# Optimization experiments

Measured on AMD Instinct MI355X. Metric: run time of the kernel, lower is better.

The kernel has to match this reference:

```python
import jax, jax.numpy as jnp
import numpy as np

HIDDEN = 896   # GRU size
HALF = HIDDEN // 2
BINS = 256     # 2 ** (16 / 2)
T = 16384      # signal length (timesteps)
INV_BINS = 1.0 / ((BINS - 1) / 2.0)


def setup_inputs() -> dict:
    key = jax.random.key(0)
    ks = jax.random.split(key, 14)
    s = 0.05
    return {
        "project_hidden_weight": jax.random.normal(ks[0], (3 * HIDDEN, HIDDEN), jnp.float32) * s,
        "project_hidden_bias": jax.random.normal(ks[1], (3 * HIDDEN,), jnp.float32) * s,
        "project_coarse_weight": jax.random.normal(ks[2], (3 * HALF, 2), jnp.float32) * s,
        "project_fine_weight": jax.random.normal(ks[3], (3 * HALF, 3), jnp.float32) * s,
        "project_coarse_bias": jax.random.normal(ks[4], (T, 3 * HALF), jnp.float32) * s,
        "project_fine_bias": jax.random.normal(ks[5], (T, 3 * HALF), jnp.float32) * s,
        "to_bins_coarse_pre_weight": jax.random.normal(ks[6], (HALF, HALF), jnp.float32) * s,
        "to_bins_coarse_pre_bias": jax.random.normal(ks[7], (HALF,), jnp.float32) * s,
        "to_bins_coarse_weight": jax.random.normal(ks[8], (BINS, HALF), jnp.float32) * s,
        "to_bins_coarse_bias": jax.random.normal(ks[9], (BINS,), jnp.float32) * s,
        "to_bins_fine_pre_weight": jax.random.normal(ks[10], (HALF, HALF), jnp.float32) * s,
        "to_bins_fine_pre_bias": jax.random.normal(ks[11], (HALF,), jnp.float32) * s,
        "to_bins_fine_weight": jax.random.normal(ks[12], (BINS, HALF), jnp.float32) * s,
        "to_bins_fine_bias": jax.random.normal(ks[13], (BINS,), jnp.float32) * s,
        "hidden_state": jnp.zeros((HIDDEN,), jnp.float32),
    }


def _half_step(inp, h, bias_t, W_in, hproj, pre_b, pre_W, bin_b, bin_W):
    # inp: [n], h: [HALF], bias_t/hproj: [3*HALF]
    proj = bias_t + W_in @ inp                               # [3*HALF]
    ri = jax.nn.sigmoid(proj[:2 * HALF] + hproj[:2 * HALF])  # r gate | u gate
    n = jnp.tanh(proj[2 * HALF:] + ri[:HALF] * hproj[2 * HALF:])
    h_new = ri[HALF:] * (h - n) + n                          # u*h + (1-u)*n
    pre = jax.nn.relu(pre_b + pre_W @ h_new)
    logits = bin_b + bin_W @ pre                             # [BINS]
    sample = jnp.argmax(logits).astype(jnp.int32)            # argmax sampling
    return h_new, sample, logits


def reference(project_hidden_weight, project_hidden_bias, project_coarse_weight,
              project_fine_weight, project_coarse_bias, project_fine_bias,
              to_bins_coarse_pre_weight, to_bins_coarse_pre_bias,
              to_bins_coarse_weight, to_bins_coarse_bias,
              to_bins_fine_pre_weight, to_bins_fine_pre_bias,
              to_bins_fine_weight, to_bins_fine_bias, hidden_state):
    init_scaled = jnp.float32((BINS // 2) * INV_BINS - 1.0)

    def step(carry, biases):
        h, c_prev, f_prev = carry
        cb, fb = biases
        hp = project_hidden_bias + project_hidden_weight @ h  # [3*HIDDEN]
        inp_c = jnp.stack([c_prev, f_prev])
        h_c, c_s, _ = _half_step(inp_c, h[:HALF], cb, project_coarse_weight,
                                 hp[:3 * HALF], to_bins_coarse_pre_bias,
                                 to_bins_coarse_pre_weight, to_bins_coarse_bias,
                                 to_bins_coarse_weight)
        c_scaled = c_s.astype(jnp.float32) * INV_BINS - 1.0
        inp_f = jnp.stack([c_prev, f_prev, c_scaled])
        h_f, f_s, _ = _half_step(inp_f, h[HALF:], fb, project_fine_weight,
                                 hp[3 * HALF:], to_bins_fine_pre_bias,
                                 to_bins_fine_pre_weight, to_bins_fine_bias,
                                 to_bins_fine_weight)
        f_scaled = f_s.astype(jnp.float32) * INV_BINS - 1.0
        return (jnp.concatenate([h_c, h_f]), c_scaled, f_scaled), (c_s, f_s)

    init = (hidden_state, init_scaled, init_scaled)
    (h_fin, _, _), (out_c, out_f) = jax.lax.scan(
        step, init, (project_coarse_bias, project_fine_bias))
    return out_c, out_f, h_fin
```

## Files before the change

### kernel.cpp

```cpp
#include <hip/hip_runtime.h>

#define AGENT __HIP_MEMORY_SCOPE_AGENT
typedef unsigned int u32;
typedef unsigned long long u64;

constexpr int TSTEPS = 16384;
constexpr float INV_BINS    = 1.0f / 127.5f;
constexpr float INIT_SCALED = 128.0f * (1.0f / 127.5f) - 1.0f;
constexpr int REP = 4;

constexpr int HT_OFF  = 0;
constexpr int HPT_OFF = 114688;
constexpr int PL_OFF  = 157696;

__device__ __forceinline__ u64  ld64(const u64* p){ return __hip_atomic_load((u64*)p, __ATOMIC_RELAXED, AGENT); }
__device__ __forceinline__ void st64(u64* p, u64 v){ __hip_atomic_store(p, v, __ATOMIC_RELAXED, AGENT); }

__device__ __forceinline__ float wave_sum(float s) {
  #pragma unroll
  for (int d = 1; d < 64; d <<= 1) s += __shfl_xor(s, d, 64);
  return s;
}
__device__ __forceinline__ u64 u64max(u64 a, u64 b) { return a > b ? a : b; }
__device__ __forceinline__ u64 wave_max64(u64 v) {
  #pragma unroll
  for (int d = 1; d < 64; d <<= 1) v = u64max(v, __shfl_xor(v, d, 64));
  return v;
}
__device__ __forceinline__ float sigf(float x) { return 1.0f / (1.0f + __expf(-x)); }
__device__ __forceinline__ u64  tagf(u32 tg, float x) { return ((u64)tg << 32) | (u64)__float_as_uint(x); }
__device__ __forceinline__ u32  tago(u64 v) { return (u32)(v >> 32); }
__device__ __forceinline__ float valf(u64 v) { return __uint_as_float((u32)(v & 0xFFFFFFFFull)); }

__device__ __forceinline__ u64 amkey(float x, int row) {
  u32 u = __float_as_uint(x);
  u = (u & 0x80000000u) ? ~u : (u | 0x80000000u);
  return ((u64)u << 8) | (u64)(u32)(255 - row);
}
__device__ __forceinline__ int amrow(u64 k) { return 255 - (int)(k & 0xFFull); }

extern "C" __global__ void __launch_bounds__(256, 1)
wavernn_persist(const float* __restrict__ Wh,  const float* __restrict__ bh,
                const float* __restrict__ Wci, const float* __restrict__ Wfi,
                const float* __restrict__ cbias, const float* __restrict__ fbias,
                const float* __restrict__ pWc, const float* __restrict__ pBc,
                const float* __restrict__ bWc, const float* __restrict__ bBc,
                const float* __restrict__ pWf, const float* __restrict__ pBf,
                const float* __restrict__ bWf, const float* __restrict__ bBf,
                const float* __restrict__ h0,
                float* __restrict__ out, char* __restrict__ wsb)
{
  const int tid  = threadIdx.x;
  const int lane = tid & 63;
  const int wv   = tid >> 6;
  const int wg   = blockIdx.x;

  u64* HT  = (u64*)(wsb + HT_OFF);
  u64* HPT = (u64*)(wsb + HPT_OFF);
  u64* PL  = (u64*)(wsb + PL_OFF);

  if (wg < 32) {
    const int half = wg >> 4;
    const int oid  = wg & 15;
    const int ncol = half ? 3 : 2;
    const float* Wi  = half ? Wfi : Wci;
    const float* tbp = half ? fbias : cbias;
    const float* pW  = half ? pWf : pWc;
    const float* pB  = half ? pBf : pBc;
    const float* bW  = half ? bWf : bWc;
    const float* bB  = half ? bBf : bBc;

    const int u1 = tid;
    const bool hasB = (tid < 192);
    const int u2 = 256 + tid;

    float wiA[3][3], wiB[3][3];
    #pragma unroll
    for (int g = 0; g < 3; ++g)
      #pragma unroll
      for (int c = 0; c < 3; ++c) {
        wiA[g][c] = (c < ncol) ? Wi[(g * 448 + u1) * ncol + c] : 0.0f;
        wiB[g][c] = (hasB && c < ncol) ? Wi[(g * 448 + u2) * ncol + c] : 0.0f;
      }
    float hvA = h0[half * 448 + u1];
    float hvB = hasB ? h0[half * 448 + u2] : 0.0f;

    float wpre[7][7], bpre[7];
    #pragma unroll
    for (int r = 0; r < 7; ++r) {
      const int row = oid * 28 + wv * 7 + r;
      #pragma unroll
      for (int k = 0; k < 7; ++k) wpre[r][k] = pW[row * 448 + k * 64 + lane];
      bpre[r] = pB[row];
    }
    float wbin[28];
    #pragma unroll
    for (int j = 0; j < 28; ++j) wbin[j] = bW[tid * 448 + oid * 28 + j];
    const float bbin = (oid == 0) ? bB[tid] : 0.0f;

    __shared__ float sh[448];
    __shared__ float spre[28];
    __shared__ u64 smA[4], smB[4], smX[4];

    for (int t = 0; t < TSTEPS; ++t) {
      const int par = t & 1;
      const u32 tg  = (u32)(t + 1);

      float tbA[3], tbB[3];
      #pragma unroll
      for (int g = 0; g < 3; ++g) {
        tbA[g] = tbp[(size_t)t * 1344 + g * 448 + u1];
        tbB[g] = hasB ? tbp[(size_t)t * 1344 + g * 448 + u2] : 0.0f;
      }

      float c_prev, f_prev;
      if (t >= 1) {
        const int parp = par ^ 1;
        const u64* plc = PL + (size_t)((parp * 2 + 0) * 16) * 256 + tid;
        const u64* plf = PL + (size_t)((parp * 2 + 1) * 16) * 256 + tid;
        float sc = 0.f, sf = 0.f;
        for (;;) {
          u64 vc[16], vf[16]; bool ok = true;
          #pragma unroll
          for (int o = 0; o < 16; ++o) { vc[o] = ld64(plc + o * 256); ok &= (tago(vc[o]) == (u32)t); }
          #pragma unroll
          for (int o = 0; o < 16; ++o) { vf[o] = ld64(plf + o * 256); ok &= (tago(vf[o]) == (u32)t); }
          if (__all(ok)) {
            sc = 0.f; sf = 0.f;
            #pragma unroll
            for (int o = 0; o < 16; ++o) { sc += valf(vc[o]); sf += valf(vf[o]); }
            break;
          }
        }
        const u64 kc = wave_max64(amkey(sc, tid));
        const u64 kf = wave_max64(amkey(sf, tid));
        if (lane == 0) { smA[wv] = kc; smB[wv] = kf; }
        __syncthreads();
        const u64 mc = u64max(u64max(smA[0], smA[1]), u64max(smA[2], smA[3]));
        const u64 mf = u64max(u64max(smB[0], smB[1]), u64max(smB[2], smB[3]));
        c_prev = (float)amrow(mc) * INV_BINS - 1.0f;
        f_prev = (float)amrow(mf) * INV_BINS - 1.0f;
        if (!half && oid == 0 && tid == 0) out[TSTEPS + t - 1] = (float)amrow(mf);
      } else {
        c_prev = INIT_SCALED; f_prev = INIT_SCALED;
      }

      const u64* hpt = HPT + (size_t)(par * 2 + half) * 1344;
      float hpA[3], hpB[3];
      for (;;) {
        u64 a0 = ld64(hpt + u1), a1 = ld64(hpt + 448 + u1), a2 = ld64(hpt + 896 + u1);
        u64 b0 = 0, b1 = 0, b2 = 0;
        bool ok = (tago(a0) == tg) && (tago(a1) == tg) && (tago(a2) == tg);
        if (hasB) {
          b0 = ld64(hpt + u2); b1 = ld64(hpt + 448 + u2); b2 = ld64(hpt + 896 + u2);
          ok &= (tago(b0) == tg) && (tago(b1) == tg) && (tago(b2) == tg);
        }
        if (__all(ok)) {
          hpA[0] = valf(a0); hpA[1] = valf(a1); hpA[2] = valf(a2);
          hpB[0] = valf(b0); hpB[1] = valf(b1); hpB[2] = valf(b2);
          break;
        }
      }

      float in2A[3], in2B[3];
      if (!half) {
        #pragma unroll
        for (int g = 0; g < 3; ++g) {
          in2A[g] = fmaf(wiA[g][1], f_prev, fmaf(wiA[g][0], c_prev, tbA[g]));
          in2B[g] = fmaf(wiB[g][1], f_prev, fmaf(wiB[g][0], c_prev, tbB[g]));
        }
      } else {
        const u64* plc = PL + (size_t)((par * 2 + 0) * 16) * 256 + tid;
        float sc2;
        for (;;) {
          u64 v[16]; bool ok = true;
          #pragma unroll
          for (int o = 0; o < 16; ++o) { v[o] = ld64(plc + o * 256); ok &= (tago(v[o]) == tg); }
          if (__all(ok)) {
            sc2 = 0.f;
            #pragma unroll
            for (int o = 0; o < 16; ++o) sc2 += valf(v[o]);
            break;
          }
        }
        const u64 k = wave_max64(amkey(sc2, tid));
        if (lane == 0) smX[wv] = k;
        __syncthreads();
        const u64 m = u64max(u64max(smX[0], smX[1]), u64max(smX[2], smX[3]));
        const int cbin = amrow(m);
        const float csc = (float)cbin * INV_BINS - 1.0f;
        if (oid == 0 && tid == 0) out[t] = (float)cbin;
        #pragma unroll
        for (int g = 0; g < 3; ++g) {
          in2A[g] = fmaf(wiA[g][2], csc, fmaf(wiA[g][1], f_prev, fmaf(wiA[g][0], c_prev, tbA[g])));
          in2B[g] = fmaf(wiB[g][2], csc, fmaf(wiB[g][1], f_prev, fmaf(wiB[g][0], c_prev, tbB[g])));
        }
      }

      {
        const float r = sigf(in2A[0] + hpA[0]);
        const float u = sigf(in2A[1] + hpA[1]);
        const float n = tanhf(in2A[2] + r * hpA[2]);
        hvA = u * (hvA - n) + n;
        sh[u1] = hvA;
        if (oid < REP) st64(HT + ((size_t)((par * 2 + half) * REP + oid)) * 448 + u1, tagf(tg, hvA));
      }
      if (hasB) {
        const float r = sigf(in2B[0] + hpB[0]);
        const float u = sigf(in2B[1] + hpB[1]);
        const float n = tanhf(in2B[2] + r * hpB[2]);
        hvB = u * (hvB - n) + n;
        sh[u2] = hvB;
        if (oid < REP) st64(HT + ((size_t)((par * 2 + half) * REP + oid)) * 448 + u2, tagf(tg, hvB));
      }
      __syncthreads();

      {
        float hv7[7];
        #pragma unroll
        for (int k = 0; k < 7; ++k) hv7[k] = sh[k * 64 + lane];
        #pragma unroll
        for (int r = 0; r < 7; ++r) {
          float s = 0.f;
          #pragma unroll
          for (int k = 0; k < 7; ++k) s = fmaf(wpre[r][k], hv7[k], s);
          s = fmaxf(wave_sum(s) + bpre[r], 0.f);
          if (lane == 0) spre[wv * 7 + r] = s;
        }
      }
      __syncthreads();

      {
        float pl = bbin;
        #pragma unroll
        for (int j = 0; j < 28; ++j) pl = fmaf(wbin[j], spre[j], pl);
        st64(PL + ((size_t)((par * 2 + half) * 16 + oid)) * 256 + tid, tagf(tg, pl));
      }
    }

    if (!half && oid == 0) {
      const u64* plf = PL + (size_t)((1 * 2 + 1) * 16) * 256 + tid;
      float sf;
      for (;;) {
        u64 v[16]; bool ok = true;
        #pragma unroll
        for (int o = 0; o < 16; ++o) { v[o] = ld64(plf + o * 256); ok &= (tago(v[o]) == 16384u); }
        if (__all(ok)) {
          sf = 0.f;
          #pragma unroll
          for (int o = 0; o < 16; ++o) sf += valf(v[o]);
          break;
        }
      }
      const u64 k = wave_max64(amkey(sf, tid));
      if (lane == 0) smA[wv] = k;
      __syncthreads();
      if (tid == 0)
        out[2 * TSTEPS - 1] =
            (float)amrow(u64max(u64max(smA[0], smA[1]), u64max(smA[2], smA[3])));
    }
    if (oid == 0) {
      out[2 * TSTEPS + half * 448 + u1] = hvA;
      if (hasB) out[2 * TSTEPS + half * 448 + u2] = hvB;
    }

  } else {
    const int id   = wg - 32;
    const int half = (id >= 42) ? 1 : 0;
    const int wgl  = id - 42 * half;
    const int r0   = (wgl * 4 + wv) * 8;
    const int rep  = wg & (REP - 1);

    float wh[8][14], hb[8];
    #pragma unroll
    for (int j = 0; j < 8; ++j) {
      const int grow = half * 1344 + r0 + j;
      #pragma unroll
      for (int k = 0; k < 14; ++k) wh[j][k] = Wh[(size_t)grow * 896 + k * 64 + lane];
      hb[j] = bh[grow];
    }

    for (int t = 0; t < TSTEPS; ++t) {
      const int par = t & 1;
      const u32 tg  = (u32)(t + 1);
      float s[8];

      if (t == 0) {
        float hv[14];
        #pragma unroll
        for (int k = 0; k < 14; ++k) hv[k] = h0[k * 64 + lane];
        #pragma unroll
        for (int j = 0; j < 8; ++j) {
          float a = 0.f;
          #pragma unroll
          for (int k = 0; k < 14; ++k) a = fmaf(wh[j][k], hv[k], a);
          s[j] = a;
        }
      } else {
        const u32 tp = (u32)t;
        const int p2 = (par ^ 1) * 2;
        const u64* hc = HT + ((size_t)((p2 + 0) * REP + rep)) * 448 + lane;
        const u64* hf = HT + ((size_t)((p2 + 1) * REP + rep)) * 448 + lane;
        {
          float hv[7];
          for (;;) {
            u64 v[7]; bool ok = true;
            #pragma unroll
            for (int k = 0; k < 7; ++k) { v[k] = ld64(hc + k * 64); ok &= (tago(v[k]) == tp); }
            if (__all(ok)) {
              #pragma unroll
              for (int k = 0; k < 7; ++k) hv[k] = valf(v[k]);
              break;
            }
          }
          #pragma unroll
          for (int j = 0; j < 8; ++j) {
            float a = 0.f;
            #pragma unroll
            for (int k = 0; k < 7; ++k) a = fmaf(wh[j][k], hv[k], a);
            s[j] = a;
          }
        }
        for (;;) { u64 sv = ld64(hf + 384); if (__all(tago(sv) == tp)) break; }
        {
          float hv[7];
          for (;;) {
            u64 v[7]; bool ok = true;
            #pragma unroll
            for (int k = 0; k < 7; ++k) { v[k] = ld64(hf + k * 64); ok &= (tago(v[k]) == tp); }
            if (__all(ok)) {
              #pragma unroll
              for (int k = 0; k < 7; ++k) hv[k] = valf(v[k]);
              break;
            }
          }
          #pragma unroll
          for (int j = 0; j < 8; ++j) {
            float a = s[j];
            #pragma unroll
            for (int k = 0; k < 7; ++k) a = fmaf(wh[j][k + 7], hv[k], a);
            s[j] = a;
          }
        }
      }

      u64* hp = HPT + (size_t)(par * 2 + half) * 1344 + r0;
      #pragma unroll
      for (int j = 0; j < 8; ++j) {
        const float a = wave_sum(s[j]) + hb[j];
        if (lane == 0) st64(hp + j, tagf(tg, a));
      }
    }
  }
}

extern "C" void kernel_launch(void* const* d_in, const int* in_sizes, int n_in,
                              void* d_out, int out_size, void* d_ws, size_t ws_size,
                              hipStream_t stream) {
  (void)in_sizes; (void)n_in; (void)out_size; (void)ws_size;
  wavernn_persist<<<116, 256, 0, stream>>>(
      (const float*)d_in[0],  (const float*)d_in[1],  (const float*)d_in[2],
      (const float*)d_in[3],  (const float*)d_in[4],  (const float*)d_in[5],
      (const float*)d_in[6],  (const float*)d_in[7],  (const float*)d_in[8],
      (const float*)d_in[9],  (const float*)d_in[10], (const float*)d_in[11],
      (const float*)d_in[12], (const float*)d_in[13], (const float*)d_in[14],
      (float*)d_out, (char*)d_ws);
}
```

Baseline: 151.1 ms.

## Centralize argmax sampling in dedicated reducer blocks publishing tagged samples

Two extra persistent workgroups now gather the per-step partial logits and compute the coarse and fine argmax. They publish the chosen bin as a tagged 64-bit value that the other 32 GRU workgroups spin on. Before, every GRU block read all 16 partial-logit slices and did its own reduction with block syncs. The partial-logit buffer is transposed so each reducer thread reads 16 contiguous entries, and the hidden-projection blocks first poll one sentinel element before loading the whole hidden vector. This cuts redundant polling and reduction traffic, at the cost of an extra global-memory hop on the serial critical path each timestep.

```diff
diff --git a/kernel.cpp b/kernel.cpp
--- a/kernel.cpp
+++ b/kernel.cpp
@@ -9,9 +9,10 @@
 constexpr float INIT_SCALED = 128.0f * (1.0f / 127.5f) - 1.0f;
 constexpr int REP = 4;
 
-constexpr int HT_OFF  = 0;
-constexpr int HPT_OFF = 114688;
-constexpr int PL_OFF  = 157696;
+constexpr int HT_OFF   = 0;
+constexpr int HPT_OFF  = 114688;
+constexpr int PL_OFF   = 157696;
+constexpr int SAMP_OFF = 288768;
 
 __device__ __forceinline__ u64  ld64(const u64* p){ return __hip_atomic_load((u64*)p, __ATOMIC_RELAXED, AGENT); }
 __device__ __forceinline__ void st64(u64* p, u64 v){ __hip_atomic_store(p, v, __ATOMIC_RELAXED, AGENT); }
@@ -55,9 +56,10 @@
   const int wv   = tid >> 6;
   const int wg   = blockIdx.x;
 
-  u64* HT  = (u64*)(wsb + HT_OFF);
-  u64* HPT = (u64*)(wsb + HPT_OFF);
-  u64* PL  = (u64*)(wsb + PL_OFF);
+  u64* HT   = (u64*)(wsb + HT_OFF);
+  u64* HPT  = (u64*)(wsb + HPT_OFF);
+  u64* PL   = (u64*)(wsb + PL_OFF);
+  u64* SAMP = (u64*)(wsb + SAMP_OFF);
 
   if (wg < 32) {
     const int half = wg >> 4;
@@ -100,7 +102,6 @@
 
     __shared__ float sh[448];
     __shared__ float spre[28];
-    __shared__ u64 smA[4], smB[4], smX[4];
 
     for (int t = 0; t < TSTEPS; ++t) {
       const int par = t & 1;
@@ -116,31 +117,15 @@
       float c_prev, f_prev;
       if (t >= 1) {
         const int parp = par ^ 1;
-        const u64* plc = PL + (size_t)((parp * 2 + 0) * 16) * 256 + tid;
-        const u64* plf = PL + (size_t)((parp * 2 + 1) * 16) * 256 + tid;
-        float sc = 0.f, sf = 0.f;
+        const u64* sc = SAMP + (size_t)((parp * 2 + 0) * 8 + (wg & 7)) * 16;
+        const u64* sf = SAMP + (size_t)((parp * 2 + 1) * 8 + (wg & 7)) * 16;
+        u64 a, b;
         for (;;) {
-          u64 vc[16], vf[16]; bool ok = true;
-          #pragma unroll
-          for (int o = 0; o < 16; ++o) { vc[o] = ld64(plc + o * 256); ok &= (tago(vc[o]) == (u32)t); }
-          #pragma unroll
-          for (int o = 0; o < 16; ++o) { vf[o] = ld64(plf + o * 256); ok &= (tago(vf[o]) == (u32)t); }
-          if (__all(ok)) {
-            sc = 0.f; sf = 0.f;
-            #pragma unroll
-            for (int o = 0; o < 16; ++o) { sc += valf(vc[o]); sf += valf(vf[o]); }
-            break;
-          }
-        }
-        const u64 kc = wave_max64(amkey(sc, tid));
-        const u64 kf = wave_max64(amkey(sf, tid));
-        if (lane == 0) { smA[wv] = kc; smB[wv] = kf; }
-        __syncthreads();
-        const u64 mc = u64max(u64max(smA[0], smA[1]), u64max(smA[2], smA[3]));
-        const u64 mf = u64max(u64max(smB[0], smB[1]), u64max(smB[2], smB[3]));
-        c_prev = (float)amrow(mc) * INV_BINS - 1.0f;
-        f_prev = (float)amrow(mf) * INV_BINS - 1.0f;
-        if (!half && oid == 0 && tid == 0) out[TSTEPS + t - 1] = (float)amrow(mf);
+          a = ld64(sc); b = ld64(sf);
+          if (__all(tago(a) == (u32)t && tago(b) == (u32)t)) break;
+        }
+        c_prev = (float)(u32)(a & 0xFFFFFFFFull) * INV_BINS - 1.0f;
+        f_prev = (float)(u32)(b & 0xFFFFFFFFull) * INV_BINS - 1.0f;
       } else {
         c_prev = INIT_SCALED; f_prev = INIT_SCALED;
       }
@@ -170,30 +155,20 @@
           in2B[g] = fmaf(wiB[g][1], f_prev, fmaf(wiB[g][0], c_prev, tbB[g]));
         }
       } else {
-        const u64* plc = PL + (size_t)((par * 2 + 0) * 16) * 256 + tid;
-        float sc2;
-        for (;;) {
-          u64 v[16]; bool ok = true;
-          #pragma unroll
-          for (int o = 0; o < 16; ++o) { v[o] = ld64(plc + o * 256); ok &= (tago(v[o]) == tg); }
-          if (__all(ok)) {
-            sc2 = 0.f;
-            #pragma unroll
-            for (int o = 0; o < 16; ++o) sc2 += valf(v[o]);
-            break;
-          }
-        }
-        const u64 k = wave_max64(amkey(sc2, tid));
-        if (lane == 0) smX[wv] = k;
-        __syncthreads();
-        const u64 m = u64max(u64max(smX[0], smX[1]), u64max(smX[2], smX[3]));
-        const int cbin = amrow(m);
-        const float csc = (float)cbin * INV_BINS - 1.0f;
-        if (oid == 0 && tid == 0) out[t] = (float)cbin;
+        float linA[3], linB[3];
         #pragma unroll
         for (int g = 0; g < 3; ++g) {
-          in2A[g] = fmaf(wiA[g][2], csc, fmaf(wiA[g][1], f_prev, fmaf(wiA[g][0], c_prev, tbA[g])));
-          in2B[g] = fmaf(wiB[g][2], csc, fmaf(wiB[g][1], f_prev, fmaf(wiB[g][0], c_prev, tbB[g])));
+          linA[g] = fmaf(wiA[g][1], f_prev, fmaf(wiA[g][0], c_prev, tbA[g]));
+          linB[g] = fmaf(wiB[g][1], f_prev, fmaf(wiB[g][0], c_prev, tbB[g]));
+        }
+        const u64* scH = SAMP + (size_t)((par * 2 + 0) * 8 + (oid & 7)) * 16;
+        u64 v;
+        for (;;) { v = ld64(scH); if (__all(tago(v) == tg)) break; }
+        const float csc = (float)(u32)(v & 0xFFFFFFFFull) * INV_BINS - 1.0f;
+        #pragma unroll
+        for (int g = 0; g < 3; ++g) {
+          in2A[g] = fmaf(wiA[g][2], csc, linA[g]);
+          in2B[g] = fmaf(wiB[g][2], csc, linB[g]);
         }
       }
 
@@ -234,34 +209,46 @@
         float pl = bbin;
         #pragma unroll
         for (int j = 0; j < 28; ++j) pl = fmaf(wbin[j], spre[j], pl);
-        st64(PL + ((size_t)((par * 2 + half) * 16 + oid)) * 256 + tid, tagf(tg, pl));
-      }
-    }
-
-    if (!half && oid == 0) {
-      const u64* plf = PL + (size_t)((1 * 2 + 1) * 16) * 256 + tid;
-      float sf;
-      for (;;) {
-        u64 v[16]; bool ok = true;
-        #pragma unroll
-        for (int o = 0; o < 16; ++o) { v[o] = ld64(plf + o * 256); ok &= (tago(v[o]) == 16384u); }
-        if (__all(ok)) {
-          sf = 0.f;
-          #pragma unroll
-          for (int o = 0; o < 16; ++o) sf += valf(v[o]);
-          break;
-        }
-      }
-      const u64 k = wave_max64(amkey(sf, tid));
-      if (lane == 0) smA[wv] = k;
-      __syncthreads();
-      if (tid == 0)
-        out[2 * TSTEPS - 1] =
-            (float)amrow(u64max(u64max(smA[0], smA[1]), u64max(smA[2], smA[3])));
-    }
+        st64(PL + ((size_t)((par * 2 + half) * 256 + tid)) * 16 + oid, tagf(tg, pl));
+      }
+    }
+
     if (oid == 0) {
       out[2 * TSTEPS + half * 448 + u1] = hvA;
       if (hasB) out[2 * TSTEPS + half * 448 + u2] = hvB;
+    }
+
+  } else if (wg >= 116) {
+    const int half = wg - 116;
+    __shared__ u64 sm2[4];
+    for (int t = 0; t < TSTEPS; ++t) {
+      const int par = t & 1;
+      const u32 tg  = (u32)(t + 1);
+      const u64* base = PL + ((size_t)((par * 2 + half) * 256 + tid)) * 16;
+      float s;
+      for (;;) {
+        u64 v0 = ld64(base);
+        if (!__all(tago(v0) == tg)) continue;
+        u64 v[16]; bool ok = true;
+        v[0] = v0;
+        #pragma unroll
+        for (int o = 1; o < 16; ++o) { v[o] = ld64(base + o); ok &= (tago(v[o]) == tg); }
+        if (__all(ok)) {
+          s = 0.f;
+          #pragma unroll
+          for (int o = 0; o < 16; ++o) s += valf(v[o]);
+          break;
+        }
+      }
+      const u64 k = wave_max64(amkey(s, tid));
+      if (lane == 0) sm2[wv] = k;
+      __syncthreads();
+      const u64 m = u64max(u64max(sm2[0], sm2[1]), u64max(sm2[2], sm2[3]));
+      const int bin = amrow(m);
+      if (tid < 8) st64(SAMP + (size_t)((par * 2 + half) * 8 + tid) * 16,
+                        ((u64)tg << 32) | (u32)bin);
+      if (tid == 0) out[half ? (TSTEPS + t) : t] = (float)bin;
+      __syncthreads();
     }
 
   } else {
@@ -301,6 +288,7 @@
         const int p2 = (par ^ 1) * 2;
         const u64* hc = HT + ((size_t)((p2 + 0) * REP + rep)) * 448 + lane;
         const u64* hf = HT + ((size_t)((p2 + 1) * REP + rep)) * 448 + lane;
+        for (;;) { u64 sv = ld64(hc + 384); if (__all(tago(sv) == tp)) break; }
         {
           float hv[7];
           for (;;) {
@@ -358,7 +346,7 @@
                               void* d_out, int out_size, void* d_ws, size_t ws_size,
                               hipStream_t stream) {
   (void)in_sizes; (void)n_in; (void)out_size; (void)ws_size;
-  wavernn_persist<<<116, 256, 0, stream>>>(
+  wavernn_persist<<<118, 256, 0, stream>>>(
       (const float*)d_in[0],  (const float*)d_in[1],  (const float*)d_in[2],
       (const float*)d_in[3],  (const float*)d_in[4],  (const float*)d_in[5],
       (const float*)d_in[6],  (const float*)d_in[7],  (const float*)d_in[8],
```

Result: slower. 219.3 ms (+45.1%).

## Reduce spin-wait contention with sentinel polling, replicated handoff buffers, and register-held coarse sample

Applied to the files above, without the earlier changes.

Polling loops now first spin on a single sentinel word per lane, with s_sleep backoff, before doing the full tagged-vector load. This is meant to cut global memory traffic and contention while blocks wait on each other. The hidden-state replicas go from 4 to 8, and the projected-hidden buffer is duplicated so each pair of workgroups polls its own copy. The fine half reuses its previous coarse sample from a register instead of re-reading and re-reducing the coarse logits, and it precomputes the input terms that do not depend on the current coarse sample. In exchange, the workspace is larger, there are more writers per step, and the sleeps can add wake-up latency.

```diff
diff --git a/kernel.cpp b/kernel.cpp
--- a/kernel.cpp
+++ b/kernel.cpp
@@ -7,11 +7,11 @@
 constexpr int TSTEPS = 16384;
 constexpr float INV_BINS    = 1.0f / 127.5f;
 constexpr float INIT_SCALED = 128.0f * (1.0f / 127.5f) - 1.0f;
-constexpr int REP = 4;
+constexpr int REP = 8;
 
 constexpr int HT_OFF  = 0;
-constexpr int HPT_OFF = 114688;
-constexpr int PL_OFF  = 157696;
+constexpr int HPT_OFF = 229376;
+constexpr int PL_OFF  = 315392;
 
 __device__ __forceinline__ u64  ld64(const u64* p){ return __hip_atomic_load((u64*)p, __ATOMIC_RELAXED, AGENT); }
 __device__ __forceinline__ void st64(u64* p, u64 v){ __hip_atomic_store(p, v, __ATOMIC_RELAXED, AGENT); }
@@ -98,12 +98,16 @@
     for (int j = 0; j < 28; ++j) wbin[j] = bW[tid * 448 + oid * 28 + j];
     const float bbin = (oid == 0) ? bB[tid] : 0.0f;
 
+    const int sidx = (tid & 15) * 256 + tid;
+
     __shared__ float sh[448];
     __shared__ float spre[28];
     __shared__ u64 smA[4], smB[4], smX[4];
 
+    float c_reg = INIT_SCALED;
+
     for (int t = 0; t < TSTEPS; ++t) {
-      const int par = t & 1;
+      const int par = t & 1, parp = par ^ 1;
       const u32 tg  = (u32)(t + 1);
 
       float tbA[3], tbB[3];
@@ -115,38 +119,73 @@
 
       float c_prev, f_prev;
       if (t >= 1) {
-        const int parp = par ^ 1;
-        const u64* plc = PL + (size_t)((parp * 2 + 0) * 16) * 256 + tid;
-        const u64* plf = PL + (size_t)((parp * 2 + 1) * 16) * 256 + tid;
-        float sc = 0.f, sf = 0.f;
-        for (;;) {
-          u64 vc[16], vf[16]; bool ok = true;
-          #pragma unroll
-          for (int o = 0; o < 16; ++o) { vc[o] = ld64(plc + o * 256); ok &= (tago(vc[o]) == (u32)t); }
-          #pragma unroll
-          for (int o = 0; o < 16; ++o) { vf[o] = ld64(plf + o * 256); ok &= (tago(vf[o]) == (u32)t); }
-          if (__all(ok)) {
-            sc = 0.f; sf = 0.f;
-            #pragma unroll
-            for (int o = 0; o < 16; ++o) { sc += valf(vc[o]); sf += valf(vf[o]); }
-            break;
-          }
-        }
-        const u64 kc = wave_max64(amkey(sc, tid));
-        const u64 kf = wave_max64(amkey(sf, tid));
-        if (lane == 0) { smA[wv] = kc; smB[wv] = kf; }
-        __syncthreads();
-        const u64 mc = u64max(u64max(smA[0], smA[1]), u64max(smA[2], smA[3]));
-        const u64 mf = u64max(u64max(smB[0], smB[1]), u64max(smB[2], smB[3]));
-        c_prev = (float)amrow(mc) * INV_BINS - 1.0f;
-        f_prev = (float)amrow(mf) * INV_BINS - 1.0f;
-        if (!half && oid == 0 && tid == 0) out[TSTEPS + t - 1] = (float)amrow(mf);
+        const u64* pc = PL + (size_t)(parp * 2 + 0) * 16 * 256;
+        const u64* pf = PL + (size_t)(parp * 2 + 1) * 16 * 256;
+        if (!half) {
+          for (;;) {
+            u64 a = ld64(pc + sidx), b = ld64(pf + sidx);
+            if (__all(tago(a) == (u32)t && tago(b) == (u32)t)) break;
+            __builtin_amdgcn_s_sleep(1);
+          }
+          float sc, sf;
+          for (;;) {
+            u64 vc[16], vf[16]; bool ok = true;
+            #pragma unroll
+            for (int o = 0; o < 16; ++o) { vc[o] = ld64(pc + o * 256 + tid); ok &= (tago(vc[o]) == (u32)t); }
+            #pragma unroll
+            for (int o = 0; o < 16; ++o) { vf[o] = ld64(pf + o * 256 + tid); ok &= (tago(vf[o]) == (u32)t); }
+            if (__all(ok)) {
+              sc = 0.f; sf = 0.f;
+              #pragma unroll
+              for (int o = 0; o < 16; ++o) { sc += valf(vc[o]); sf += valf(vf[o]); }
+              break;
+            }
+          }
+          const u64 kc = wave_max64(amkey(sc, tid));
+          const u64 kf = wave_max64(amkey(sf, tid));
+          if (lane == 0) { smA[wv] = kc; smB[wv] = kf; }
+          __syncthreads();
+          const u64 mc = u64max(u64max(smA[0], smA[1]), u64max(smA[2], smA[3]));
+          const u64 mf = u64max(u64max(smB[0], smB[1]), u64max(smB[2], smB[3]));
+          c_prev = (float)amrow(mc) * INV_BINS - 1.0f;
+          f_prev = (float)amrow(mf) * INV_BINS - 1.0f;
+          if (oid == 0 && tid == 0) out[TSTEPS + t - 1] = (float)amrow(mf);
+        } else {
+          c_prev = c_reg;
+          for (;;) {
+            u64 b = ld64(pf + sidx);
+            if (__all(tago(b) == (u32)t)) break;
+            __builtin_amdgcn_s_sleep(1);
+          }
+          float sf;
+          for (;;) {
+            u64 vf[16]; bool ok = true;
+            #pragma unroll
+            for (int o = 0; o < 16; ++o) { vf[o] = ld64(pf + o * 256 + tid); ok &= (tago(vf[o]) == (u32)t); }
+            if (__all(ok)) {
+              sf = 0.f;
+              #pragma unroll
+              for (int o = 0; o < 16; ++o) sf += valf(vf[o]);
+              break;
+            }
+          }
+          const u64 kf = wave_max64(amkey(sf, tid));
+          if (lane == 0) smB[wv] = kf;
+          __syncthreads();
+          const u64 mf = u64max(u64max(smB[0], smB[1]), u64max(smB[2], smB[3]));
+          f_prev = (float)amrow(mf) * INV_BINS - 1.0f;
+        }
       } else {
         c_prev = INIT_SCALED; f_prev = INIT_SCALED;
       }
 
-      const u64* hpt = HPT + (size_t)(par * 2 + half) * 1344;
+      const u64* hpt = HPT + (size_t)((par * 2 + half) * 2 + (wg & 1)) * 1344;
       float hpA[3], hpB[3];
+      for (;;) {
+        bool ok = (tago(ld64(hpt + u1)) == tg);
+        if (hasB) ok &= (tago(ld64(hpt + u2)) == tg);
+        if (__all(ok)) break;
+      }
       for (;;) {
         u64 a0 = ld64(hpt + u1), a1 = ld64(hpt + 448 + u1), a2 = ld64(hpt + 896 + u1);
         u64 b0 = 0, b1 = 0, b2 = 0;
@@ -170,12 +209,21 @@
           in2B[g] = fmaf(wiB[g][1], f_prev, fmaf(wiB[g][0], c_prev, tbB[g]));
         }
       } else {
-        const u64* plc = PL + (size_t)((par * 2 + 0) * 16) * 256 + tid;
+        float linA[3], linB[3];
+        #pragma unroll
+        for (int g = 0; g < 3; ++g) {
+          linA[g] = fmaf(wiA[g][1], f_prev, fmaf(wiA[g][0], c_prev, tbA[g]));
+          linB[g] = fmaf(wiB[g][1], f_prev, fmaf(wiB[g][0], c_prev, tbB[g]));
+        }
+        const u64* pcb = PL + (size_t)(par * 2 + 0) * 16 * 256;
+        for (;;) {
+          if (__all(tago(ld64(pcb + sidx)) == tg)) break;
+        }
         float sc2;
         for (;;) {
           u64 v[16]; bool ok = true;
           #pragma unroll
-          for (int o = 0; o < 16; ++o) { v[o] = ld64(plc + o * 256); ok &= (tago(v[o]) == tg); }
+          for (int o = 0; o < 16; ++o) { v[o] = ld64(pcb + o * 256 + tid); ok &= (tago(v[o]) == tg); }
           if (__all(ok)) {
             sc2 = 0.f;
             #pragma unroll
@@ -189,11 +237,12 @@
         const u64 m = u64max(u64max(smX[0], smX[1]), u64max(smX[2], smX[3]));
         const int cbin = amrow(m);
         const float csc = (float)cbin * INV_BINS - 1.0f;
+        c_reg = csc;
         if (oid == 0 && tid == 0) out[t] = (float)cbin;
         #pragma unroll
         for (int g = 0; g < 3; ++g) {
-          in2A[g] = fmaf(wiA[g][2], csc, fmaf(wiA[g][1], f_prev, fmaf(wiA[g][0], c_prev, tbA[g])));
-          in2B[g] = fmaf(wiB[g][2], csc, fmaf(wiB[g][1], f_prev, fmaf(wiB[g][0], c_prev, tbB[g])));
+          in2A[g] = fmaf(wiA[g][2], csc, linA[g]);
+          in2B[g] = fmaf(wiB[g][2], csc, linB[g]);
         }
       }
 
@@ -239,12 +288,16 @@
     }
 
     if (!half && oid == 0) {
-      const u64* plf = PL + (size_t)((1 * 2 + 1) * 16) * 256 + tid;
+      const u64* pf = PL + (size_t)(1 * 2 + 1) * 16 * 256;
+      for (;;) {
+        if (__all(tago(ld64(pf + sidx)) == 16384u)) break;
+        __builtin_amdgcn_s_sleep(1);
+      }
       float sf;
       for (;;) {
         u64 v[16]; bool ok = true;
         #pragma unroll
-        for (int o = 0; o < 16; ++o) { v[o] = ld64(plf + o * 256); ok &= (tago(v[o]) == 16384u); }
+        for (int o = 0; o < 16; ++o) { v[o] = ld64(pf + o * 256 + tid); ok &= (tago(v[o]) == 16384u); }
         if (__all(ok)) {
           sf = 0.f;
           #pragma unroll
@@ -301,6 +354,11 @@
         const int p2 = (par ^ 1) * 2;
         const u64* hc = HT + ((size_t)((p2 + 0) * REP + rep)) * 448 + lane;
         const u64* hf = HT + ((size_t)((p2 + 1) * REP + rep)) * 448 + lane;
+        for (;;) {
+          u64 sv = ld64(hc + 384);
+          if (__all(tago(sv) == tp)) break;
+          __builtin_amdgcn_s_sleep(1);
+        }
         {
           float hv[7];
           for (;;) {
@@ -344,11 +402,11 @@
         }
       }
 
-      u64* hp = HPT + (size_t)(par * 2 + half) * 1344 + r0;
       #pragma unroll
       for (int j = 0; j < 8; ++j) {
         const float a = wave_sum(s[j]) + hb[j];
-        if (lane == 0) st64(hp + j, tagf(tg, a));
+        if (lane < 2)
+          st64(HPT + (size_t)((par * 2 + half) * 2 + lane) * 1344 + r0 + j, tagf(tg, a));
       }
     }
   }
```

Measured after the change: 169.9 ms. +12.5%, slower.
